# Performance work log

Measured on AMD Instinct MI355X. Metric: run time of the kernel, lower is better.

The kernel has to match this reference:

```python
import jax, jax.numpy as jnp
import numpy as np

B, L, E, D = 4, 2048, 512, 128


def setup_inputs() -> dict:
    key = jax.random.key(0)
    k1, k2 = jax.random.split(key)
    emb_sentences = jax.random.normal(k1, (B, L, E), dtype=jnp.float32)
    # torch nn.Linear weight layout: [out_dim, in_dim]
    W = jax.random.normal(k2, (D, E), dtype=jnp.float32) * (1.0 / np.sqrt(E))
    return {"emb_sentences": emb_sentences, "W": W}


def reference(emb_sentences, W):
    # dep_embeddings = Linear(emb) with no bias: [B, L, D]
    dep = jnp.einsum('ble,de->bld', emb_sentences, W)
    # All-pairs squared Euclidean distances without the O(L^2 * D)
    # broadcast intermediate: ||xi - xj||^2 = ||xi||^2 + ||xj||^2 - 2 xi.xj
    sq = jnp.sum(dep * dep, axis=-1)                 # [B, L]
    gram = jnp.einsum('bid,bjd->bij', dep, dep)      # [B, L, L]
    distances = sq[:, :, None] + sq[:, None, :] - 2.0 * gram
    return dep, distances
```

## Files before the change

kernel.cpp:

```cpp
#include <hip/hip_runtime.h>
#include <hip/hip_bf16.h>


typedef __attribute__((ext_vector_type(8))) short  short8;
typedef __attribute__((ext_vector_type(4))) float  floatx4;
typedef __attribute__((ext_vector_type(4))) unsigned short ushortx4;

#define B_  4
#define L_  2048
#define E_  512
#define D_  128
#define M_  (B_*L_)

__device__ __forceinline__ unsigned short f2bfu(float x) {
    __hip_bfloat16 h = __float2bfloat16(x);
    union { __hip_bfloat16 h; unsigned short u; } c; c.h = h; return c.u;
}
__device__ __forceinline__ float bfu2f(unsigned short u) {
    union { unsigned u32; float f; } c; c.u32 = ((unsigned)u) << 16; return c.f;
}
__device__ __forceinline__ short8 cvt8(const float* p) {
    float4 x = *reinterpret_cast<const float4*>(p);
    float4 y = *reinterpret_cast<const float4*>(p + 4);
    short8 t;
    t[0] = (short)f2bfu(x.x); t[1] = (short)f2bfu(x.y);
    t[2] = (short)f2bfu(x.z); t[3] = (short)f2bfu(x.w);
    t[4] = (short)f2bfu(y.x); t[5] = (short)f2bfu(y.y);
    t[6] = (short)f2bfu(y.z); t[7] = (short)f2bfu(y.w);
    return t;
}

__global__ __launch_bounds__(256)
void kW(const float* __restrict__ W, unsigned short* __restrict__ Wb)
{
    int i = (blockIdx.x * 256 + threadIdx.x) * 4;
    float4 v = *reinterpret_cast<const float4*>(W + i);
    ushort4 u;
    u.x = f2bfu(v.x); u.y = f2bfu(v.y); u.z = f2bfu(v.z); u.w = f2bfu(v.w);
    *reinterpret_cast<ushort4*>(Wb + i) = u;
}

__global__ __launch_bounds__(256)
void kP1(const float* __restrict__ emb, const unsigned short* __restrict__ Wb,
         float* __restrict__ dep_out, unsigned short* __restrict__ dep_b16,
         float* __restrict__ sq)
{
    __shared__ float pws[16][4];
    const int tid  = threadIdx.x;
    const int lane = tid & 63, wave = tid >> 6;
    const int l15 = lane & 15, lg = lane >> 4;
    const long m0 = (long)blockIdx.x * 16;

    floatx4 acc[2] = { (floatx4){0.f,0.f,0.f,0.f}, (floatx4){0.f,0.f,0.f,0.f} };
    const float* ar = emb + (m0 + l15) * E_;
    const unsigned short* w0 = Wb + (wave * 32 + l15) * E_;
    const unsigned short* w1 = Wb + (wave * 32 + 16 + l15) * E_;

    #pragma unroll
    for (int k0 = 0; k0 < E_; k0 += 32) {
        const int kc = k0 + lg * 8;
        short8 bfm = cvt8(ar + kc);
        short8 af0 = *reinterpret_cast<const short8*>(w0 + kc);
        short8 af1 = *reinterpret_cast<const short8*>(w1 + kc);
        acc[0] = __builtin_amdgcn_mfma_f32_16x16x32_bf16(af0, bfm, acc[0], 0, 0, 0);
        acc[1] = __builtin_amdgcn_mfma_f32_16x16x32_bf16(af1, bfm, acc[1], 0, 0, 0);
    }

    const long m = m0 + l15;
    float p = 0.f;
    #pragma unroll
    for (int ni = 0; ni < 2; ++ni) {
        const int dbase = wave * 32 + ni * 16 + lg * 4;
        floatx4  v;
        ushortx4 u;
        #pragma unroll
        for (int j = 0; j < 4; ++j) {
            v[j] = acc[ni][j];
            u[j] = f2bfu(v[j]);
            float vb = bfu2f(u[j]);
            p += vb * vb;
        }
        *reinterpret_cast<floatx4*>(dep_out + m * D_ + dbase)  = v;
        *reinterpret_cast<ushortx4*>(dep_b16 + m * D_ + dbase) = u;
    }
    p += __shfl_xor(p, 16);
    p += __shfl_xor(p, 32);
    if (lane < 16) pws[lane][wave] = p;
    __syncthreads();
    if (tid < 16)
        sq[m0 + tid] = pws[tid][0] + pws[tid][1] + pws[tid][2] + pws[tid][3];
}

__global__ __launch_bounds__(256, 4)
void kP2(const unsigned short* __restrict__ dep_b16, const float* __restrict__ sq,
         float* __restrict__ dist)
{
    __shared__ __align__(16) unsigned short Js[128][136];

    const int tid  = threadIdx.x;
    const int lane = tid & 63;
    const int wave = tid >> 6;
    const int wr = wave >> 1, wc = wave & 1;
    const int l15 = lane & 15, lg = lane >> 4;

    const int swz = (blockIdx.x & 7) * 128 + (blockIdx.x >> 3);
    const int b  = swz >> 8;
    const int i0 = ((swz >> 4) & 15) * 128;
    const int j0 = (swz & 15) * 128;
    const unsigned short* depb = dep_b16 + (long)b * L_ * D_;

    #pragma unroll
    for (int jj = 0; jj < 8; ++jj) {
        int chunk = tid + 256 * jj;
        int row = chunk >> 4, c8 = chunk & 15;
        *reinterpret_cast<short8*>(&Js[row][c8 * 8]) =
            *reinterpret_cast<const short8*>(depb + (long)(j0 + row) * D_ + c8 * 8);
    }

    const unsigned short* ibase = depb + (long)(i0 + wr * 64 + l15) * D_ + lg * 8;

    short8 af[2][4];
    #pragma unroll
    for (int kk = 0; kk < 4; ++kk)
        af[0][kk] = *reinterpret_cast<const short8*>(ibase + kk * 32);

    const float* sqb = sq + b * L_;
    float sri[4];
    #pragma unroll
    for (int mi = 0; mi < 4; ++mi)
        sri[mi] = sqb[i0 + wr * 64 + mi * 16 + l15];
    floatx4 sqj[4];
    #pragma unroll
    for (int ni = 0; ni < 4; ++ni)
        sqj[ni] = *reinterpret_cast<const floatx4*>(sqb + j0 + wc * 64 + ni * 16 + lg * 4);

    __syncthreads();

    float* db = dist + (long)b * L_ * L_;
    #pragma unroll
    for (int mi = 0; mi < 4; ++mi) {
        if (mi < 3) {
            #pragma unroll
            for (int kk = 0; kk < 4; ++kk)
                af[(mi + 1) & 1][kk] = *reinterpret_cast<const short8*>(
                    ibase + (long)(mi + 1) * 16 * D_ + kk * 32);
        }
        floatx4 acc[4];
        #pragma unroll
        for (int ni = 0; ni < 4; ++ni)
            acc[ni] = (floatx4){0.f, 0.f, 0.f, 0.f};
        #pragma unroll
        for (int ni = 0; ni < 4; ++ni) {
            #pragma unroll
            for (int kk = 0; kk < 4; ++kk) {
                short8 bf = *reinterpret_cast<const short8*>(
                    &Js[wc * 64 + ni * 16 + l15][kk * 32 + lg * 8]);
                acc[ni] = __builtin_amdgcn_mfma_f32_16x16x32_bf16(
                    bf, af[mi & 1][kk], acc[ni], 0, 0, 0);
            }
        }
        const long i = i0 + wr * 64 + mi * 16 + l15;
        #pragma unroll
        for (int ni = 0; ni < 4; ++ni) {
            const int jb = j0 + wc * 64 + ni * 16 + lg * 4;
            floatx4 v;
            #pragma unroll
            for (int jj = 0; jj < 4; ++jj)
                v[jj] = sri[mi] + sqj[ni][jj] - 2.0f * acc[ni][jj];
            *reinterpret_cast<floatx4*>(db + i * L_ + jb) = v;
        }
    }
}

extern "C" void kernel_launch(void* const* d_in, const int* in_sizes, int n_in,
                              void* d_out, int out_size, void* d_ws, size_t ws_size,
                              hipStream_t stream)
{
    const float* emb = (const float*)d_in[0];
    const float* W   = (const float*)d_in[1];

    float* dep_out = (float*)d_out;
    float* dist    = dep_out + (size_t)M_ * D_;

    unsigned short* dep_b16 = (unsigned short*)d_ws;
    float* sq = (float*)((char*)d_ws + (size_t)M_ * D_ * sizeof(unsigned short));
    unsigned short* Wb = (unsigned short*)((char*)sq + (size_t)M_ * sizeof(float));

    hipLaunchKernelGGL(kW,  dim3((D_ * E_) / (256 * 4)), dim3(256), 0, stream, W, Wb);
    hipLaunchKernelGGL(kP1, dim3(M_ / 16), dim3(256), 0, stream,
                       emb, Wb, dep_out, dep_b16, sq);
    hipLaunchKernelGGL(kP2, dim3(16 * 16 * B_), dim3(256), 0, stream,
                       dep_b16, sq, dist);
}
```

Baseline: 49.21 us.

## Fuse projection and distance kernels into cooperative megakernel with per-batch flags

Merges the projection GEMM and the pairwise-distance GEMM into one cooperative kernel. The first 512 blocks compute dep rows and bump a per-batch atomic counter, and every block then spins until its batch's counter reaches 128 before running the distance tile. This is meant to remove the launch gap and tail idle between the two phases. Phase 1 is also restructured: each wave now takes a K-slice and computes all 128 outputs, and the waves reduce through shared memory. The change adds a memset, spin-wait overhead and a fallback path with two separate launches if the cooperative launch fails.

```diff
diff --git a/kernel.cpp b/kernel.cpp
--- a/kernel.cpp
+++ b/kernel.cpp
@@ -4,13 +4,14 @@
 
 typedef __attribute__((ext_vector_type(8))) short  short8;
 typedef __attribute__((ext_vector_type(4))) float  floatx4;
-typedef __attribute__((ext_vector_type(4))) unsigned short ushortx4;
 
 #define B_  4
 #define L_  2048
 #define E_  512
 #define D_  128
 #define M_  (B_*L_)
+#define NPROD 512
+#define NBLK  1024
 
 __device__ __forceinline__ unsigned short f2bfu(float x) {
     __hip_bfloat16 h = __float2bfloat16(x);
@@ -40,73 +41,89 @@
     *reinterpret_cast<ushort4*>(Wb + i) = u;
 }
 
-__global__ __launch_bounds__(256)
-void kP1(const float* __restrict__ emb, const unsigned short* __restrict__ Wb,
-         float* __restrict__ dep_out, unsigned short* __restrict__ dep_b16,
-         float* __restrict__ sq)
-{
-    __shared__ float pws[16][4];
-    const int tid  = threadIdx.x;
-    const int lane = tid & 63, wave = tid >> 6;
+__device__ __forceinline__ void phase1(int bid, int tid,
+    const float* __restrict__ emb, const unsigned short* __restrict__ Wb,
+    float* __restrict__ dep_out, unsigned short* __restrict__ dep_b16,
+    float* __restrict__ sq, char* smem)
+{
+    float (*sc)[16][132] = reinterpret_cast<float (*)[16][132]>(smem);
+    const int lane = tid & 63, w = tid >> 6;
     const int l15 = lane & 15, lg = lane >> 4;
-    const long m0 = (long)blockIdx.x * 16;
-
-    floatx4 acc[2] = { (floatx4){0.f,0.f,0.f,0.f}, (floatx4){0.f,0.f,0.f,0.f} };
-    const float* ar = emb + (m0 + l15) * E_;
-    const unsigned short* w0 = Wb + (wave * 32 + l15) * E_;
-    const unsigned short* w1 = Wb + (wave * 32 + 16 + l15) * E_;
-
-    #pragma unroll
-    for (int k0 = 0; k0 < E_; k0 += 32) {
+    const long m0 = (long)bid * 16;
+
+    floatx4 acc[8];
+    #pragma unroll
+    for (int dg = 0; dg < 8; ++dg) acc[dg] = (floatx4){0.f, 0.f, 0.f, 0.f};
+
+    const float* ar = emb + (m0 + l15) * E_ + w * 128;
+    const unsigned short* wb = Wb + l15 * E_ + w * 128;
+
+    #pragma unroll
+    for (int k0 = 0; k0 < 128; k0 += 32) {
         const int kc = k0 + lg * 8;
         short8 bfm = cvt8(ar + kc);
-        short8 af0 = *reinterpret_cast<const short8*>(w0 + kc);
-        short8 af1 = *reinterpret_cast<const short8*>(w1 + kc);
-        acc[0] = __builtin_amdgcn_mfma_f32_16x16x32_bf16(af0, bfm, acc[0], 0, 0, 0);
-        acc[1] = __builtin_amdgcn_mfma_f32_16x16x32_bf16(af1, bfm, acc[1], 0, 0, 0);
-    }
-
-    const long m = m0 + l15;
+        #pragma unroll
+        for (int dg = 0; dg < 8; ++dg) {
+            short8 af = *reinterpret_cast<const short8*>(wb + dg * 16 * E_ + kc);
+            acc[dg] = __builtin_amdgcn_mfma_f32_16x16x32_bf16(af, bfm, acc[dg], 0, 0, 0);
+        }
+    }
+    #pragma unroll
+    for (int dg = 0; dg < 8; ++dg)
+        *reinterpret_cast<floatx4*>(&sc[w][l15][dg * 16 + lg * 4]) = acc[dg];
+    __syncthreads();
+
+    const int r = tid >> 4, i = tid & 15;
+    const long m = m0 + r;
     float p = 0.f;
-    #pragma unroll
-    for (int ni = 0; ni < 2; ++ni) {
-        const int dbase = wave * 32 + ni * 16 + lg * 4;
-        floatx4  v;
-        ushortx4 u;
-        #pragma unroll
-        for (int j = 0; j < 4; ++j) {
-            v[j] = acc[ni][j];
-            u[j] = f2bfu(v[j]);
-            float vb = bfu2f(u[j]);
+    short8 u8;
+    #pragma unroll
+    for (int h = 0; h < 2; ++h) {
+        floatx4 v = *reinterpret_cast<const floatx4*>(&sc[0][r][i * 8 + h * 4]);
+        v += *reinterpret_cast<const floatx4*>(&sc[1][r][i * 8 + h * 4]);
+        v += *reinterpret_cast<const floatx4*>(&sc[2][r][i * 8 + h * 4]);
+        v += *reinterpret_cast<const floatx4*>(&sc[3][r][i * 8 + h * 4]);
+        *reinterpret_cast<floatx4*>(dep_out + m * D_ + i * 8 + h * 4) = v;
+        #pragma unroll
+        for (int c = 0; c < 4; ++c) {
+            unsigned short u = f2bfu(v[c]);
+            u8[h * 4 + c] = (short)u;
+            float vb = bfu2f(u);
             p += vb * vb;
         }
-        *reinterpret_cast<floatx4*>(dep_out + m * D_ + dbase)  = v;
-        *reinterpret_cast<ushortx4*>(dep_b16 + m * D_ + dbase) = u;
-    }
-    p += __shfl_xor(p, 16);
-    p += __shfl_xor(p, 32);
-    if (lane < 16) pws[lane][wave] = p;
+    }
+    *reinterpret_cast<short8*>(dep_b16 + m * D_ + i * 8) = u8;
+    p += __shfl_xor(p, 1); p += __shfl_xor(p, 2);
+    p += __shfl_xor(p, 4); p += __shfl_xor(p, 8);
+    if (i == 0) sq[m] = p;
     __syncthreads();
-    if (tid < 16)
-        sq[m0 + tid] = pws[tid][0] + pws[tid][1] + pws[tid][2] + pws[tid][3];
-}
-
-__global__ __launch_bounds__(256, 4)
-void kP2(const unsigned short* __restrict__ dep_b16, const float* __restrict__ sq,
-         float* __restrict__ dist)
-{
-    __shared__ __align__(16) unsigned short Js[128][136];
-
-    const int tid  = threadIdx.x;
+}
+
+__device__ __forceinline__ void phase2(int bidx, int tid,
+    const unsigned short* __restrict__ dep_b16, const float* __restrict__ sq,
+    float* __restrict__ dist, int* flags, char* smem)
+{
+    unsigned short (*Js)[136] = reinterpret_cast<unsigned short (*)[136]>(smem);
+
     const int lane = tid & 63;
     const int wave = tid >> 6;
     const int wr = wave >> 1, wc = wave & 1;
     const int l15 = lane & 15, lg = lane >> 4;
 
-    const int swz = (blockIdx.x & 7) * 128 + (blockIdx.x >> 3);
+    const int swz = (bidx & 7) * 128 + (bidx >> 3);
     const int b  = swz >> 8;
     const int i0 = ((swz >> 4) & 15) * 128;
     const int j0 = (swz & 15) * 128;
+
+    if (flags) {
+        if (tid == 0) {
+            while (__hip_atomic_load(flags + b, __ATOMIC_ACQUIRE,
+                                     __HIP_MEMORY_SCOPE_AGENT) < 128)
+                __builtin_amdgcn_s_sleep(8);
+        }
+        __syncthreads();
+    }
+
     const unsigned short* depb = dep_b16 + (long)b * L_ * D_;
 
     #pragma unroll
@@ -118,7 +135,6 @@
     }
 
     const unsigned short* ibase = depb + (long)(i0 + wr * 64 + l15) * D_ + lg * 8;
-
     short8 af[2][4];
     #pragma unroll
     for (int kk = 0; kk < 4; ++kk)
@@ -172,6 +188,39 @@
     }
 }
 
+__global__ __launch_bounds__(256, 4)
+void kMega(const float* __restrict__ emb, const unsigned short* __restrict__ Wb,
+           float* __restrict__ dep_out, unsigned short* __restrict__ dep_b16,
+           float* __restrict__ sq, float* __restrict__ dist, int* flags)
+{
+    __shared__ __align__(16) char smem[34816];
+    const int bid = blockIdx.x, tid = threadIdx.x;
+    if (bid < NPROD) {
+        phase1(bid, tid, emb, Wb, dep_out, dep_b16, sq, smem);
+        if (tid == 0)
+            __hip_atomic_fetch_add(flags + (bid >> 7), 1, __ATOMIC_RELEASE,
+                                   __HIP_MEMORY_SCOPE_AGENT);
+    }
+    phase2(bid, tid, dep_b16, sq, dist, flags, smem);
+}
+
+__global__ __launch_bounds__(256)
+void kP1s(const float* __restrict__ emb, const unsigned short* __restrict__ Wb,
+          float* __restrict__ dep_out, unsigned short* __restrict__ dep_b16,
+          float* __restrict__ sq)
+{
+    __shared__ __align__(16) char smem[33792];
+    phase1(blockIdx.x, threadIdx.x, emb, Wb, dep_out, dep_b16, sq, smem);
+}
+
+__global__ __launch_bounds__(256, 4)
+void kP2s(const unsigned short* __restrict__ dep_b16, const float* __restrict__ sq,
+          float* __restrict__ dist)
+{
+    __shared__ __align__(16) char smem[34816];
+    phase2(blockIdx.x, threadIdx.x, dep_b16, sq, dist, nullptr, smem);
+}
+
 extern "C" void kernel_launch(void* const* d_in, const int* in_sizes, int n_in,
                               void* d_out, int out_size, void* d_ws, size_t ws_size,
                               hipStream_t stream)
@@ -182,13 +231,24 @@
     float* dep_out = (float*)d_out;
     float* dist    = dep_out + (size_t)M_ * D_;
 
-    unsigned short* dep_b16 = (unsigned short*)d_ws;
-    float* sq = (float*)((char*)d_ws + (size_t)M_ * D_ * sizeof(unsigned short));
-    unsigned short* Wb = (unsigned short*)((char*)sq + (size_t)M_ * sizeof(float));
-
-    hipLaunchKernelGGL(kW,  dim3((D_ * E_) / (256 * 4)), dim3(256), 0, stream, W, Wb);
-    hipLaunchKernelGGL(kP1, dim3(M_ / 16), dim3(256), 0, stream,
-                       emb, Wb, dep_out, dep_b16, sq);
-    hipLaunchKernelGGL(kP2, dim3(16 * 16 * B_), dim3(256), 0, stream,
-                       dep_b16, sq, dist);
-}
+    char* ws = (char*)d_ws;
+    unsigned short* dep_b16 = (unsigned short*)ws;            ws += (size_t)M_ * D_ * 2;
+    float* sq               = (float*)ws;                     ws += (size_t)M_ * 4;
+    unsigned short* Wb      = (unsigned short*)ws;            ws += (size_t)D_ * E_ * 2;
+    int* flags              = (int*)ws;
+
+    hipMemsetAsync(flags, 0, B_ * sizeof(int), stream);
+    hipLaunchKernelGGL(kW, dim3((D_ * E_) / (256 * 4)), dim3(256), 0, stream, W, Wb);
+
+    void* args[7] = { (void*)&emb, (void*)&Wb, (void*)&dep_out,
+                      (void*)&dep_b16, (void*)&sq, (void*)&dist, (void*)&flags };
+    hipError_t err = hipLaunchCooperativeKernel((const void*)kMega,
+                                                dim3(NBLK), dim3(256),
+                                                args, 0, stream);
+    if (err != hipSuccess) {
+        hipLaunchKernelGGL(kP1s, dim3(NPROD), dim3(256), 0, stream,
+                           emb, Wb, dep_out, dep_b16, sq);
+        hipLaunchKernelGGL(kP2s, dim3(NBLK), dim3(256), 0, stream,
+                           dep_b16, sq, dist);
+    }
+}
```

Result: slower. 153.4 us (+211.8%).
